# Kernel optimization log

Measured on AMD Instinct MI355X. Metric: run time of the kernel, lower is better.

Reference implementation:

```python
import jax, jax.numpy as jnp
import numpy as np

NUM_HOPS = 3
SIGMA = 0.1
EPS = 1e-12  # torch F.normalize default eps


def _l2_normalize(v):
    n = jnp.linalg.norm(v, axis=1, keepdims=True)
    return v / jnp.maximum(n, EPS)


def setup_inputs() -> dict:
    key = jax.random.key(0)
    k1, k2 = jax.random.split(key)
    N, d, E = 50000, 128, 500000
    x = jax.random.normal(k1, (N, d), dtype=jnp.float32)
    edge_index = jax.random.randint(k2, (2, E), 0, N, dtype=jnp.int64)
    return {"x": x, "edge_index": edge_index}


def reference(x, edge_index):
    N = x.shape[0]
    src, dst = edge_index[0], edge_index[1]
    noise_key = jax.random.key(42)
    h = _l2_normalize(x)
    outs = [h]
    for k in range(NUM_HOPS):
        h_src = h[src]                              # [E, d] gather
        h_dst = h[dst]                              # [E, d] gather
        alpha = jax.nn.sigmoid(jnp.sum(h_src * h_dst, axis=1))  # [E]
        # sparse.mm(alpha^T, h): out[dst] += alpha_e * h[src]
        aggr = jax.ops.segment_sum(alpha[:, None] * h_src, dst, num_segments=N)
        noise = SIGMA * jax.random.normal(jax.random.fold_in(noise_key, k), aggr.shape, aggr.dtype)
        h = _l2_normalize(aggr + noise)
        outs.append(h)
    return jnp.stack(outs)  # [num_hops+1, N, d]
```

## Files before the change

### kernel.cpp

```cpp
#include <hip/hip_runtime.h>
#include <stdint.h>

#define D 128
#define SIGMA 0.1f

typedef unsigned int uint;
typedef unsigned short ushort;

#if __has_builtin(__builtin_amdgcn_fdot2_f32_bf16)
#define HAVE_DOT2 1
typedef __bf16 bf16x2 __attribute__((ext_vector_type(2)));
__device__ inline float dot2b(uint a, uint b, float c) {
  union { uint u; bf16x2 v; } ua, ub;
  ua.u = a; ub.u = b;
  return __builtin_amdgcn_fdot2_f32_bf16(ua.v, ub.v, c, false);
}
#else
#define HAVE_DOT2 0
#endif

typedef float v2f __attribute__((ext_vector_type(2)));

__host__ __device__ inline void tf2x32(uint32_t k0, uint32_t k1,
                                       uint32_t x0, uint32_t x1,
                                       uint32_t& o0, uint32_t& o1) {
  const uint32_t ks2 = k0 ^ k1 ^ 0x1BD11BDAu;
#define ROTL(v, r) (((v) << (r)) | ((v) >> (32 - (r))))
#define RND(R) { x0 += x1; x1 = ROTL(x1, R); x1 ^= x0; }
  x0 += k0; x1 += k1;
  RND(13) RND(15) RND(26) RND(6)
  x0 += k1; x1 += ks2 + 1u;
  RND(17) RND(29) RND(16) RND(24)
  x0 += ks2; x1 += k0 + 2u;
  RND(13) RND(15) RND(26) RND(6)
  x0 += k0; x1 += k1 + 3u;
  RND(17) RND(29) RND(16) RND(24)
  x0 += k1; x1 += ks2 + 4u;
  RND(13) RND(15) RND(26) RND(6)
  x0 += ks2; x1 += k0 + 5u;
#undef RND
#undef ROTL
  o0 = x0; o1 = x1;
}

__device__ inline float jax_normal_pu(uint32_t k0, uint32_t k1, uint32_t idx) {
  uint32_t o0, o1;
  tf2x32(k0, k1, 0u, idx, o0, o1);
  uint32_t bits = o0 ^ o1;
  float f = __uint_as_float((bits >> 9) | 0x3f800000u) - 1.0f;
  const float lo = __uint_as_float(0xBF7FFFFFu);
  float u = fmaxf(lo, f * 2.0f + lo);
  float w = -__logf((1.0f - u) * (1.0f + u));
  float p;
  if (w < 5.0f) {
    w -= 2.5f;
    p = 2.81022636e-08f;
    p = fmaf(p, w, 3.43273939e-07f);
    p = fmaf(p, w, -3.5233877e-06f);
    p = fmaf(p, w, -4.39150654e-06f);
    p = fmaf(p, w, 0.00021858087f);
    p = fmaf(p, w, -0.00125372503f);
    p = fmaf(p, w, -0.00417768164f);
    p = fmaf(p, w, 0.246640727f);
    p = fmaf(p, w, 1.50140941f);
  } else {
    w = sqrtf(w) - 3.0f;
    p = -0.000200214257f;
    p = fmaf(p, w, 0.000100950558f);
    p = fmaf(p, w, 0.00134934322f);
    p = fmaf(p, w, -0.00367342844f);
    p = fmaf(p, w, 0.00573950773f);
    p = fmaf(p, w, -0.0076224613f);
    p = fmaf(p, w, 0.00943887047f);
    p = fmaf(p, w, 1.00167406f);
    p = fmaf(p, w, 2.83297682f);
  }
  return p * u;
}
#define NOISE_SCALE 0.14142135624f

__device__ inline uint bf16r(float f) {
  uint u = __float_as_uint(f);
  return (u + 0x7fffu + ((u >> 16) & 1u)) >> 16;
}

__device__ inline void unpk8(uint4 u, float* a) {
  a[0] = __uint_as_float(u.x << 16);
  a[1] = __uint_as_float(u.x & 0xffff0000u);
  a[2] = __uint_as_float(u.y << 16);
  a[3] = __uint_as_float(u.y & 0xffff0000u);
  a[4] = __uint_as_float(u.z << 16);
  a[5] = __uint_as_float(u.z & 0xffff0000u);
  a[6] = __uint_as_float(u.w << 16);
  a[7] = __uint_as_float(u.w & 0xffff0000u);
}

__device__ inline void unpk8v(uint4 u, v2f* a) {
  a[0] = v2f{__uint_as_float(u.x << 16), __uint_as_float(u.x & 0xffff0000u)};
  a[1] = v2f{__uint_as_float(u.y << 16), __uint_as_float(u.y & 0xffff0000u)};
  a[2] = v2f{__uint_as_float(u.z << 16), __uint_as_float(u.z & 0xffff0000u)};
  a[3] = v2f{__uint_as_float(u.w << 16), __uint_as_float(u.w & 0xffff0000u)};
}

template<int USEB>
__device__ inline void ldrow16(const float* __restrict__ hf,
                               const uint4* __restrict__ hb,
                               int node, int sl, float* a) {
  if (USEB) {
    unpk8(hb[node * 16 + sl], a);
  } else {
    float4 v0 = ((const float4*)hf)[node * 32 + sl * 2];
    float4 v1 = ((const float4*)hf)[node * 32 + sl * 2 + 1];
    a[0] = v0.x; a[1] = v0.y; a[2] = v0.z; a[3] = v0.w;
    a[4] = v1.x; a[5] = v1.y; a[6] = v1.z; a[7] = v1.w;
  }
}

__global__ __launch_bounds__(256) void k_zero(int4* __restrict__ p, int n4) {
  int i = blockIdx.x * blockDim.x + threadIdx.x;
  if (i < n4) p[i] = make_int4(0, 0, 0, 0);
}

__global__ __launch_bounds__(256) void k_hist(const int* __restrict__ dst,
                                              int* __restrict__ cnt, int E) {
  int i = (blockIdx.x * blockDim.x + threadIdx.x) * 4;
  if (i + 3 < E) {
    int4 d = *(const int4*)(dst + i);
    atomicAdd(&cnt[d.x], 1);
    atomicAdd(&cnt[d.y], 1);
    atomicAdd(&cnt[d.z], 1);
    atomicAdd(&cnt[d.w], 1);
  } else {
    for (int j = i; j < E; ++j) atomicAdd(&cnt[dst[j]], 1);
  }
}

__global__ __launch_bounds__(256) void k_bsum(const int* __restrict__ cnt,
                                              int* __restrict__ bsum, int N) {
  __shared__ int ws[4];
  int b = blockIdx.x, t = threadIdx.x;
  int base = b * 1024 + t * 4;
  int4 c = {0, 0, 0, 0};
  if (base + 3 < N) c = *(const int4*)(cnt + base);
  else {
    if (base < N) c.x = cnt[base];
    if (base + 1 < N) c.y = cnt[base + 1];
    if (base + 2 < N) c.z = cnt[base + 2];
    if (base + 3 < N) c.w = cnt[base + 3];
  }
  int s = c.x + c.y + c.z + c.w;
  #pragma unroll
  for (int off = 32; off; off >>= 1) s += __shfl_xor(s, off);
  if ((t & 63) == 0) ws[t >> 6] = s;
  __syncthreads();
  if (t == 0) bsum[b] = ws[0] + ws[1] + ws[2] + ws[3];
}

__global__ __launch_bounds__(256) void k_apply2(const int* __restrict__ cnt,
                                                const int* __restrict__ bsum,
                                                int* __restrict__ row,
                                                int* __restrict__ cur,
                                                int N, int NB) {
  __shared__ int sboff;
  __shared__ int wsum[4];
  int b = blockIdx.x, t = threadIdx.x;
  if (t < 64) {
    int v = (t < NB) ? bsum[t] : 0;
    int incl = v;
    #pragma unroll
    for (int off = 1; off < 64; off <<= 1) {
      int tv = __shfl_up(incl, off);
      if (t >= off) incl += tv;
    }
    if (t == b) sboff = incl - v;
    if (b == 0 && t == NB - 1) row[N] = incl;
  }
  __syncthreads();

  int base = b * 1024 + t * 4;
  int4 c = {0, 0, 0, 0};
  if (base + 3 < N) c = *(const int4*)(cnt + base);
  else {
    if (base < N) c.x = cnt[base];
    if (base + 1 < N) c.y = cnt[base + 1];
    if (base + 2 < N) c.z = cnt[base + 2];
    if (base + 3 < N) c.w = cnt[base + 3];
  }
  int s = c.x + c.y + c.z + c.w;
  int incl = s;
  #pragma unroll
  for (int off = 1; off < 64; off <<= 1) {
    int tv = __shfl_up(incl, off);
    if ((t & 63) >= off) incl += tv;
  }
  int wid = t >> 6;
  if ((t & 63) == 63) wsum[wid] = incl;
  __syncthreads();
  int woff = 0;
  for (int w = 0; w < wid; ++w) woff += wsum[w];
  int ex = sboff + woff + incl - s;
  int r0 = ex, r1 = ex + c.x, r2 = r1 + c.y, r3 = r2 + c.z;
  if (base + 3 < N) {
    *(int4*)(row + base) = make_int4(r0, r1, r2, r3);
    *(int4*)(cur + base) = make_int4(r0, r1, r2, r3);
  } else {
    if (base < N)     { row[base] = r0;     cur[base] = r0; }
    if (base + 1 < N) { row[base + 1] = r1; cur[base + 1] = r1; }
    if (base + 2 < N) { row[base + 2] = r2; cur[base + 2] = r2; }
  }
}

__global__ void k_bscan(const int* __restrict__ bsum, int* __restrict__ boff,
                        int* __restrict__ rowN, int NB) {
  int lane = threadIdx.x;
  int carry = 0;
  for (int base = 0; base < NB; base += 64) {
    int idx = base + lane;
    int v = (idx < NB) ? bsum[idx] : 0;
    int incl = v;
    #pragma unroll
    for (int off = 1; off < 64; off <<= 1) {
      int t = __shfl_up(incl, off);
      if (lane >= off) incl += t;
    }
    if (idx < NB) boff[idx] = carry + incl - v;
    carry += __shfl(incl, 63);
  }
  if (lane == 0) rowN[0] = carry;
}

__global__ __launch_bounds__(256) void k_apply(const int* __restrict__ cnt,
                                               const int* __restrict__ boff,
                                               int* __restrict__ row,
                                               int* __restrict__ cur, int N) {
  __shared__ int wsum[4];
  int b = blockIdx.x, t = threadIdx.x;
  int base = b * 1024 + t * 4;
  int4 c = {0, 0, 0, 0};
  if (base + 3 < N) c = *(const int4*)(cnt + base);
  else {
    if (base < N) c.x = cnt[base];
    if (base + 1 < N) c.y = cnt[base + 1];
    if (base + 2 < N) c.z = cnt[base + 2];
    if (base + 3 < N) c.w = cnt[base + 3];
  }
  int s = c.x + c.y + c.z + c.w;
  int incl = s;
  #pragma unroll
  for (int off = 1; off < 64; off <<= 1) {
    int tv = __shfl_up(incl, off);
    if ((t & 63) >= off) incl += tv;
  }
  int wid = t >> 6;
  if ((t & 63) == 63) wsum[wid] = incl;
  __syncthreads();
  int woff = 0;
  for (int w = 0; w < wid; ++w) woff += wsum[w];
  int ex = boff[b] + woff + incl - s;
  int r0 = ex, r1 = ex + c.x, r2 = r1 + c.y, r3 = r2 + c.z;
  if (base + 3 < N) {
    *(int4*)(row + base) = make_int4(r0, r1, r2, r3);
    *(int4*)(cur + base) = make_int4(r0, r1, r2, r3);
  } else {
    if (base < N)     { row[base] = r0;     cur[base] = r0; }
    if (base + 1 < N) { row[base + 1] = r1; cur[base + 1] = r1; }
    if (base + 2 < N) { row[base + 2] = r2; cur[base + 2] = r2; }
  }
}

__global__ __launch_bounds__(256) void k_fill(const int* __restrict__ src,
                                              const int* __restrict__ dst,
                                              int* __restrict__ cur,
                                              int* __restrict__ csr, int E) {
  int i = (blockIdx.x * blockDim.x + threadIdx.x) * 4;
  if (i + 3 < E) {
    int4 d = *(const int4*)(dst + i);
    int4 s = *(const int4*)(src + i);
    csr[atomicAdd(&cur[d.x], 1)] = s.x;
    csr[atomicAdd(&cur[d.y], 1)] = s.y;
    csr[atomicAdd(&cur[d.z], 1)] = s.z;
    csr[atomicAdd(&cur[d.w], 1)] = s.w;
  } else {
    for (int j = i; j < E; ++j) csr[atomicAdd(&cur[dst[j]], 1)] = src[j];
  }
}

template<int USEB>
__global__ __launch_bounds__(256) void k_norm0(const float* __restrict__ x,
                                               float* __restrict__ h,
                                               uint2* __restrict__ hb, int N) {
  int gid = blockIdx.x * blockDim.x + threadIdx.x;
  int node = gid >> 5, lane = gid & 31;
  if (node >= N) return;
  float4 v = ((const float4*)x)[node * 32 + lane];
  float ss = v.x * v.x + v.y * v.y + v.z * v.z + v.w * v.w;
  #pragma unroll
  for (int off = 16; off; off >>= 1) ss += __shfl_xor(ss, off);
  float inv = 1.0f / fmaxf(sqrtf(ss), 1e-12f);
  float4 o; o.x = v.x * inv; o.y = v.y * inv; o.z = v.z * inv; o.w = v.w * inv;
  ((float4*)h)[node * 32 + lane] = o;
  if (USEB) {
    uint2 u;
    u.x = bf16r(o.x) | (bf16r(o.y) << 16);
    u.y = bf16r(o.z) | (bf16r(o.w) << 16);
    hb[node * 32 + lane] = u;
  }
}

template<int USEB>
__global__ __launch_bounds__(256) void k_hop(
    const float* __restrict__ hpf, const uint4* __restrict__ hpb,
    float* __restrict__ hof, uint* __restrict__ hob, int wb,
    const int* __restrict__ row, const int* __restrict__ csr,
    int N, uint32_t k0, uint32_t k1) {
  int gid = blockIdx.x * blockDim.x + threadIdx.x;
  int node = gid >> 6;
  if (node >= N) return;
  int lane = threadIdx.x & 63;
  int sl = lane & 15, g = lane >> 4;

  int b = __builtin_amdgcn_readfirstlane(row[node]);
  int e = __builtin_amdgcn_readfirstlane(row[node + 1]);

  uint32_t j0 = (uint32_t)node * 128u + (uint32_t)sl * 8u + (uint32_t)g * 2u;
  float n0 = jax_normal_pu(k0, k1, j0);
  float n1 = jax_normal_pu(k0, k1, j0 + 1u);

#if HAVE_DOT2
  if (USEB) {
    uint4 hvp = hpb[node * 16 + sl];
    v2f acc[4] = {v2f{0.f,0.f}, v2f{0.f,0.f}, v2f{0.f,0.f}, v2f{0.f,0.f}};

    for (int cb = b; cb < e; cb += 64) {
      int cn = min(64, e - cb);
      int eidx = csr[min(cb + lane, e - 1)];
      for (int jb = 0; jb < cn; jb += 16) {
        int rem = cn - jb;
        uint4 u0, u1, u2, u3;
        {
          int i0 = __shfl(eidx, jb + g);
          u0 = hpb[i0 * 16 + sl];
        }
        if (rem > 4)  { int i1 = __shfl(eidx, jb + 4 + g);  u1 = hpb[i1 * 16 + sl]; }
        if (rem > 8)  { int i2 = __shfl(eidx, jb + 8 + g);  u2 = hpb[i2 * 16 + sl]; }
        if (rem > 12) { int i3 = __shfl(eidx, jb + 12 + g); u3 = hpb[i3 * 16 + sl]; }

        #define PROC(UU, SBASE)                                                 \
        {                                                                       \
          float p = dot2b(UU.w, hvp.w, dot2b(UU.z, hvp.z,                       \
                    dot2b(UU.y, hvp.y, dot2b(UU.x, hvp.x, 0.f))));              \
          p += __shfl_xor(p, 1);                                                \
          p += __shfl_xor(p, 2);                                                \
          p += __shfl_xor(p, 4);                                                \
          p += __shfl_xor(p, 8);                                                \
          float al = ((SBASE) + g < rem)                                        \
                       ? __builtin_amdgcn_rcpf(1.0f + __expf(-p)) : 0.f;        \
          v2f a[4]; v2f vv = v2f{al, al};                                       \
          unpk8v(UU, a);                                                        \
          acc[0] = __builtin_elementwise_fma(vv, a[0], acc[0]);                 \
          acc[1] = __builtin_elementwise_fma(vv, a[1], acc[1]);                 \
          acc[2] = __builtin_elementwise_fma(vv, a[2], acc[2]);                 \
          acc[3] = __builtin_elementwise_fma(vv, a[3], acc[3]);                 \
        }
        PROC(u0, 0)
        if (rem > 4)  PROC(u1, 4)
        if (rem > 8)  PROC(u2, 8)
        if (rem > 12) PROC(u3, 12)
        #undef PROC
      }
    }

    float ac[8] = {acc[0][0], acc[0][1], acc[1][0], acc[1][1],
                   acc[2][0], acc[2][1], acc[3][0], acc[3][1]};
    #pragma unroll
    for (int t = 0; t < 8; ++t) {
      ac[t] += __shfl_xor(ac[t], 16);
      ac[t] += __shfl_xor(ac[t], 32);
    }
    float p0s = (g & 1) ? ac[2] : ac[0];
    float p1s = (g & 1) ? ac[3] : ac[1];
    float q0s = (g & 1) ? ac[6] : ac[4];
    float q1s = (g & 1) ? ac[7] : ac[5];
    float s0 = (g & 2) ? q0s : p0s;
    float s1 = (g & 2) ? q1s : p1s;

    s0 += NOISE_SCALE * n0;
    s1 += NOISE_SCALE * n1;

    float ss = s0 * s0 + s1 * s1;
    #pragma unroll
    for (int off = 32; off; off >>= 1) ss += __shfl_xor(ss, off);
    float inv = __builtin_amdgcn_rcpf(fmaxf(sqrtf(ss), 1e-12f));
    float o0 = s0 * inv, o1 = s1 * inv;
    int oi = node * 64 + sl * 4 + g;
    ((float2*)hof)[oi] = make_float2(o0, o1);
    if (wb) hob[oi] = bf16r(o0) | (bf16r(o1) << 16);
    return;
  }
#endif

  float hv[8];
  ldrow16<USEB>(hpf, hpb, node, sl, hv);
  float acc[8] = {0.f, 0.f, 0.f, 0.f, 0.f, 0.f, 0.f, 0.f};
  for (int cb = b; cb < e; cb += 64) {
    int cn = min(64, e - cb);
    int eidx = csr[min(cb + lane, e - 1)];
    for (int jb = 0; jb < cn; jb += 16) {
      int pos = jb + (g << 2);
      int i0 = __shfl(eidx, pos);
      int i1 = __shfl(eidx, pos + 1);
      int i2 = __shfl(eidx, pos + 2);
      int i3 = __shfl(eidx, pos + 3);
      float a0[8], a1[8], a2[8], a3[8];
      ldrow16<USEB>(hpf, hpb, i0, sl, a0);
      ldrow16<USEB>(hpf, hpb, i1, sl, a1);
      ldrow16<USEB>(hpf, hpb, i2, sl, a2);
      ldrow16<USEB>(hpf, hpb, i3, sl, a3);
      float p0 = 0.f, p1 = 0.f, p2 = 0.f, p3 = 0.f;
      #pragma unroll
      for (int t = 0; t < 8; ++t) {
        p0 = fmaf(a0[t], hv[t], p0);
        p1 = fmaf(a1[t], hv[t], p1);
        p2 = fmaf(a2[t], hv[t], p2);
        p3 = fmaf(a3[t], hv[t], p3);
      }
      #pragma unroll
      for (int off = 1; off < 16; off <<= 1) {
        p0 += __shfl_xor(p0, off);
        p1 += __shfl_xor(p1, off);
        p2 += __shfl_xor(p2, off);
        p3 += __shfl_xor(p3, off);
      }
      float al0 = (pos     < cn) ? __builtin_amdgcn_rcpf(1.0f + __expf(-p0)) : 0.f;
      float al1 = (pos + 1 < cn) ? __builtin_amdgcn_rcpf(1.0f + __expf(-p1)) : 0.f;
      float al2 = (pos + 2 < cn) ? __builtin_amdgcn_rcpf(1.0f + __expf(-p2)) : 0.f;
      float al3 = (pos + 3 < cn) ? __builtin_amdgcn_rcpf(1.0f + __expf(-p3)) : 0.f;
      #pragma unroll
      for (int t = 0; t < 8; ++t) {
        acc[t] = fmaf(al0, a0[t], acc[t]);
        acc[t] = fmaf(al1, a1[t], acc[t]);
        acc[t] = fmaf(al2, a2[t], acc[t]);
        acc[t] = fmaf(al3, a3[t], acc[t]);
      }
    }
  }
  #pragma unroll
  for (int t = 0; t < 8; ++t) {
    acc[t] += __shfl_xor(acc[t], 16);
    acc[t] += __shfl_xor(acc[t], 32);
  }
  float p0s = (g & 1) ? acc[2] : acc[0];
  float p1s = (g & 1) ? acc[3] : acc[1];
  float q0s = (g & 1) ? acc[6] : acc[4];
  float q1s = (g & 1) ? acc[7] : acc[5];
  float s0 = (g & 2) ? q0s : p0s;
  float s1 = (g & 2) ? q1s : p1s;

  s0 += NOISE_SCALE * n0;
  s1 += NOISE_SCALE * n1;

  float ss = s0 * s0 + s1 * s1;
  #pragma unroll
  for (int off = 32; off; off >>= 1) ss += __shfl_xor(ss, off);
  float inv = __builtin_amdgcn_rcpf(fmaxf(sqrtf(ss), 1e-12f));
  float o0 = s0 * inv, o1 = s1 * inv;
  int oi = node * 64 + sl * 4 + g;
  ((float2*)hof)[oi] = make_float2(o0, o1);
  if (USEB && wb) hob[oi] = bf16r(o0) | (bf16r(o1) << 16);
}

extern "C" void kernel_launch(void* const* d_in, const int* in_sizes, int n_in,
                              void* d_out, int out_size, void* d_ws, size_t ws_size,
                              hipStream_t stream) {
  const float* x = (const float*)d_in[0];
  const int* ei = (const int*)d_in[1];
  int N = in_sizes[0] / D;
  int E = in_sizes[1] / 2;
  const int* src = ei;
  const int* dst = ei + E;
  float* out = (float*)d_out;
  size_t nd = (size_t)N * D;

  int Np = (N + 3) & ~3;
  int Ep = (E + 3) & ~3;
  int NB = (N + 1023) / 1024;
  int NBp = (NB + 3) & ~3;
  int* cnt  = (int*)d_ws;
  int* row  = cnt + Np;
  int* cur  = row + Np + 4;
  int* csr  = cur + Np;
  int* bsum = csr + Ep;
  int* boff = bsum + NBp;

  size_t int_bytes = ((size_t)(3 * Np + 4 + Ep + 2 * NBp)) * 4;
  size_t hb_off = (int_bytes + 255) & ~(size_t)255;
  size_t hb_bytes = (size_t)N * D * 2;
  bool useb = ws_size >= hb_off + 2 * hb_bytes;
  ushort* hb0 = (ushort*)((char*)d_ws + hb_off);
  ushort* hb1 = hb0 + (size_t)N * D;

  int n4 = Np / 4;
  k_zero<<<(n4 + 255) / 256, 256, 0, stream>>>((int4*)cnt, n4);
  int eb4 = (E / 4 + 256) / 256;
  k_hist<<<eb4, 256, 0, stream>>>(dst, cnt, E);
  k_bsum<<<NB, 256, 0, stream>>>(cnt, bsum, N);
  if (NB <= 64) {
    k_apply2<<<NB, 256, 0, stream>>>(cnt, bsum, row, cur, N, NB);
  } else {
    k_bscan<<<1, 64, 0, stream>>>(bsum, boff, row + N, NB);
    k_apply<<<NB, 256, 0, stream>>>(cnt, boff, row, cur, N);
  }
  k_fill<<<eb4, 256, 0, stream>>>(src, dst, cur, csr, E);

  int nb32 = (N * 32 + 255) / 256;
  int nb64 = (N * 64 + 255) / 256;

  if (useb) {
    k_norm0<1><<<nb32, 256, 0, stream>>>(x, out, (uint2*)hb0, N);
    for (int k = 0; k < 3; ++k) {
      uint32_t ka, kb;
      tf2x32(0u, 42u, 0u, (uint32_t)k, ka, kb);
      const uint4* hin = (const uint4*)((k & 1) ? hb1 : hb0);
      uint* hout = (uint*)((k & 1) ? hb0 : hb1);
      k_hop<1><<<nb64, 256, 0, stream>>>(nullptr, hin,
                                         out + (size_t)(k + 1) * nd, hout,
                                         (k < 2) ? 1 : 0,
                                         row, csr, N, ka, kb);
    }
  } else {
    k_norm0<0><<<nb32, 256, 0, stream>>>(x, out, nullptr, N);
    for (int k = 0; k < 3; ++k) {
      uint32_t ka, kb;
      tf2x32(0u, 42u, 0u, (uint32_t)k, ka, kb);
      k_hop<0><<<nb64, 256, 0, stream>>>(out + (size_t)k * nd, nullptr,
                                         out + (size_t)(k + 1) * nd, nullptr, 0,
                                         row, csr, N, ka, kb);
    }
  }
}
```

Measured before the change: 169.7 us.

## Precompute hop noise in preprocessing kernels and batch edge gathers with DPP reductions

The Gaussian noise for all three hops is now generated in extra blocks appended to the histogram, fill and norm0 launches. It is stored as bf16 in workspace, so the hop kernels only load it instead of running Threefry and erfinv inline. The hop edge loop is restructured into templated batches that issue all gathers before the dot products, and part of the dot-product reduction uses DPP moves instead of shuffles. The trade-offs are extra workspace traffic and bf16 rounding of the noise, which adds a small accuracy risk.

```diff
diff --git a/kernel.cpp b/kernel.cpp
--- a/kernel.cpp
+++ b/kernel.cpp
@@ -3,6 +3,7 @@
 
 #define D 128
 #define SIGMA 0.1f
+#define NOISE_SCALE 0.14142135624f
 
 typedef unsigned int uint;
 typedef unsigned short ushort;
@@ -17,6 +18,17 @@
 }
 #else
 #define HAVE_DOT2 0
+#endif
+
+#if __has_builtin(__builtin_amdgcn_mov_dpp)
+#define HAVE_DPP 1
+template<int CTRL>
+__device__ inline float dppadd(float x) {
+  int v = __builtin_amdgcn_mov_dpp(__float_as_int(x), CTRL, 0xF, 0xF, true);
+  return x + __int_as_float(v);
+}
+#else
+#define HAVE_DPP 0
 #endif
 
 typedef float v2f __attribute__((ext_vector_type(2)));
@@ -77,22 +89,10 @@
   }
   return p * u;
 }
-#define NOISE_SCALE 0.14142135624f
 
 __device__ inline uint bf16r(float f) {
   uint u = __float_as_uint(f);
   return (u + 0x7fffu + ((u >> 16) & 1u)) >> 16;
-}
-
-__device__ inline void unpk8(uint4 u, float* a) {
-  a[0] = __uint_as_float(u.x << 16);
-  a[1] = __uint_as_float(u.x & 0xffff0000u);
-  a[2] = __uint_as_float(u.y << 16);
-  a[3] = __uint_as_float(u.y & 0xffff0000u);
-  a[4] = __uint_as_float(u.z << 16);
-  a[5] = __uint_as_float(u.z & 0xffff0000u);
-  a[6] = __uint_as_float(u.w << 16);
-  a[7] = __uint_as_float(u.w & 0xffff0000u);
 }
 
 __device__ inline void unpk8v(uint4 u, v2f* a) {
@@ -102,18 +102,11 @@
   a[3] = v2f{__uint_as_float(u.w << 16), __uint_as_float(u.w & 0xffff0000u)};
 }
 
-template<int USEB>
-__device__ inline void ldrow16(const float* __restrict__ hf,
-                               const uint4* __restrict__ hb,
-                               int node, int sl, float* a) {
-  if (USEB) {
-    unpk8(hb[node * 16 + sl], a);
-  } else {
-    float4 v0 = ((const float4*)hf)[node * 32 + sl * 2];
-    float4 v1 = ((const float4*)hf)[node * 32 + sl * 2 + 1];
-    a[0] = v0.x; a[1] = v0.y; a[2] = v0.z; a[3] = v0.w;
-    a[4] = v1.x; a[5] = v1.y; a[6] = v1.z; a[7] = v1.w;
-  }
+__device__ inline void gen_noise(uint* __restrict__ nb, int t, uint ka, uint kb) {
+  uint j0 = (uint)(t >> 6) * 128u + (uint)(t & 15) * 8u + (uint)((t >> 4) & 3) * 2u;
+  float a = jax_normal_pu(ka, kb, j0);
+  float b = jax_normal_pu(ka, kb, j0 + 1u);
+  nb[t] = bf16r(a) | (bf16r(b) << 16);
 }
 
 __global__ __launch_bounds__(256) void k_zero(int4* __restrict__ p, int n4) {
@@ -121,9 +114,9 @@
   if (i < n4) p[i] = make_int4(0, 0, 0, 0);
 }
 
-__global__ __launch_bounds__(256) void k_hist(const int* __restrict__ dst,
-                                              int* __restrict__ cnt, int E) {
-  int i = (blockIdx.x * blockDim.x + threadIdx.x) * 4;
+__device__ inline void hist_body(const int* __restrict__ dst, int* __restrict__ cnt,
+                                 int E, int bx, int tx) {
+  int i = (bx * 256 + tx) * 4;
   if (i + 3 < E) {
     int4 d = *(const int4*)(dst + i);
     atomicAdd(&cnt[d.x], 1);
@@ -133,6 +126,56 @@
   } else {
     for (int j = i; j < E; ++j) atomicAdd(&cnt[dst[j]], 1);
   }
+}
+
+__device__ inline void fill_body(const int* __restrict__ src, const int* __restrict__ dst,
+                                 int* __restrict__ cur, int* __restrict__ csr,
+                                 int E, int bx, int tx) {
+  int i = (bx * 256 + tx) * 4;
+  if (i + 3 < E) {
+    int4 d = *(const int4*)(dst + i);
+    int4 s = *(const int4*)(src + i);
+    csr[atomicAdd(&cur[d.x], 1)] = s.x;
+    csr[atomicAdd(&cur[d.y], 1)] = s.y;
+    csr[atomicAdd(&cur[d.z], 1)] = s.z;
+    csr[atomicAdd(&cur[d.w], 1)] = s.w;
+  } else {
+    for (int j = i; j < E; ++j) csr[atomicAdd(&cur[dst[j]], 1)] = src[j];
+  }
+}
+
+__global__ __launch_bounds__(256) void k_hist(const int* __restrict__ dst,
+                                              int* __restrict__ cnt, int E) {
+  hist_body(dst, cnt, E, blockIdx.x, threadIdx.x);
+}
+
+__global__ __launch_bounds__(256) void k_hist_noise(const int* __restrict__ dst,
+                                                    int* __restrict__ cnt, int E, int HB,
+                                                    uint* __restrict__ nb, int NT,
+                                                    uint ka, uint kb) {
+  int bx = blockIdx.x;
+  if (bx < HB) { hist_body(dst, cnt, E, bx, threadIdx.x); return; }
+  int t = (bx - HB) * 256 + threadIdx.x;
+  if (t < NT) gen_noise(nb, t, ka, kb);
+}
+
+__global__ __launch_bounds__(256) void k_fill(const int* __restrict__ src,
+                                              const int* __restrict__ dst,
+                                              int* __restrict__ cur,
+                                              int* __restrict__ csr, int E) {
+  fill_body(src, dst, cur, csr, E, blockIdx.x, threadIdx.x);
+}
+
+__global__ __launch_bounds__(256) void k_fill_noise(const int* __restrict__ src,
+                                                    const int* __restrict__ dst,
+                                                    int* __restrict__ cur,
+                                                    int* __restrict__ csr, int E, int FB,
+                                                    uint* __restrict__ nb, int NT,
+                                                    uint ka, uint kb) {
+  int bx = blockIdx.x;
+  if (bx < FB) { fill_body(src, dst, cur, csr, E, bx, threadIdx.x); return; }
+  int t = (bx - FB) * 256 + threadIdx.x;
+  if (t < NT) gen_noise(nb, t, ka, kb);
 }
 
 __global__ __launch_bounds__(256) void k_bsum(const int* __restrict__ cnt,
@@ -268,28 +311,9 @@
   }
 }
 
-__global__ __launch_bounds__(256) void k_fill(const int* __restrict__ src,
-                                              const int* __restrict__ dst,
-                                              int* __restrict__ cur,
-                                              int* __restrict__ csr, int E) {
-  int i = (blockIdx.x * blockDim.x + threadIdx.x) * 4;
-  if (i + 3 < E) {
-    int4 d = *(const int4*)(dst + i);
-    int4 s = *(const int4*)(src + i);
-    csr[atomicAdd(&cur[d.x], 1)] = s.x;
-    csr[atomicAdd(&cur[d.y], 1)] = s.y;
-    csr[atomicAdd(&cur[d.z], 1)] = s.z;
-    csr[atomicAdd(&cur[d.w], 1)] = s.w;
-  } else {
-    for (int j = i; j < E; ++j) csr[atomicAdd(&cur[dst[j]], 1)] = src[j];
-  }
-}
-
-template<int USEB>
-__global__ __launch_bounds__(256) void k_norm0(const float* __restrict__ x,
-                                               float* __restrict__ h,
-                                               uint2* __restrict__ hb, int N) {
-  int gid = blockIdx.x * blockDim.x + threadIdx.x;
+__device__ inline void norm0_body(const float* __restrict__ x, float* __restrict__ h,
+                                  uint2* __restrict__ hb, int N, int bx, int tx) {
+  int gid = bx * 256 + tx;
   int node = gid >> 5, lane = gid & 31;
   if (node >= N) return;
   float4 v = ((const float4*)x)[node * 32 + lane];
@@ -299,7 +323,7 @@
   float inv = 1.0f / fmaxf(sqrtf(ss), 1e-12f);
   float4 o; o.x = v.x * inv; o.y = v.y * inv; o.z = v.z * inv; o.w = v.w * inv;
   ((float4*)h)[node * 32 + lane] = o;
-  if (USEB) {
+  if (hb) {
     uint2 u;
     u.x = bf16r(o.x) | (bf16r(o.y) << 16);
     u.y = bf16r(o.z) | (bf16r(o.w) << 16);
@@ -307,10 +331,150 @@
   }
 }
 
-template<int USEB>
-__global__ __launch_bounds__(256) void k_hop(
-    const float* __restrict__ hpf, const uint4* __restrict__ hpb,
+__global__ __launch_bounds__(256) void k_norm0(const float* __restrict__ x,
+                                               float* __restrict__ h,
+                                               uint2* __restrict__ hb, int N) {
+  norm0_body(x, h, hb, N, blockIdx.x, threadIdx.x);
+}
+
+__global__ __launch_bounds__(256) void k_norm0_noise(const float* __restrict__ x,
+                                                     float* __restrict__ h,
+                                                     uint2* __restrict__ hb, int N, int NB0,
+                                                     uint* __restrict__ nb, int NT,
+                                                     uint ka, uint kb) {
+  int bx = blockIdx.x;
+  if (bx < NB0) { norm0_body(x, h, hb, N, bx, threadIdx.x); return; }
+  int t = (bx - NB0) * 256 + threadIdx.x;
+  if (t < NT) gen_noise(nb, t, ka, kb);
+}
+
+#if HAVE_DOT2
+template<int K, bool M>
+__device__ inline void edge_body(int jb, int rem, int eidx,
+                                 const uint4* __restrict__ hpb,
+                                 uint4 hvp, int sl, int g, v2f* acc) {
+  uint4 u[K];
+  #pragma unroll
+  for (int j = 0; j < K; ++j) {
+    int idx = __shfl(eidx, jb + 4 * j + g);
+    u[j] = hpb[idx * 16 + sl];
+  }
+  float p[K];
+  #pragma unroll
+  for (int j = 0; j < K; ++j)
+    p[j] = dot2b(u[j].w, hvp.w, dot2b(u[j].z, hvp.z,
+            dot2b(u[j].y, hvp.y, dot2b(u[j].x, hvp.x, 0.f))));
+#if HAVE_DPP
+  #pragma unroll
+  for (int j = 0; j < K; ++j) p[j] = dppadd<0xB1>(p[j]);
+  #pragma unroll
+  for (int j = 0; j < K; ++j) p[j] = dppadd<0x4E>(p[j]);
+  #pragma unroll
+  for (int j = 0; j < K; ++j) p[j] += __shfl_xor(p[j], 4);
+  #pragma unroll
+  for (int j = 0; j < K; ++j) p[j] += __shfl_xor(p[j], 8);
+#else
+  #pragma unroll
+  for (int off = 1; off < 16; off <<= 1) {
+    #pragma unroll
+    for (int j = 0; j < K; ++j) p[j] += __shfl_xor(p[j], off);
+  }
+#endif
+  float al[K];
+  #pragma unroll
+  for (int j = 0; j < K; ++j) {
+    bool ok = (!M) || (j < K - 1) || (4 * (K - 1) + g < rem);
+    al[j] = ok ? __builtin_amdgcn_rcpf(1.0f + __expf(-p[j])) : 0.f;
+  }
+  #pragma unroll
+  for (int j = 0; j < K; ++j) {
+    v2f a[4]; unpk8v(u[j], a);
+    v2f vv = v2f{al[j], al[j]};
+    acc[0] = __builtin_elementwise_fma(vv, a[0], acc[0]);
+    acc[1] = __builtin_elementwise_fma(vv, a[1], acc[1]);
+    acc[2] = __builtin_elementwise_fma(vv, a[2], acc[2]);
+    acc[3] = __builtin_elementwise_fma(vv, a[3], acc[3]);
+  }
+}
+
+template<int PRE>
+__global__ __launch_bounds__(256) void k_hop2(
+    const uint4* __restrict__ hpb,
     float* __restrict__ hof, uint* __restrict__ hob, int wb,
+    const int* __restrict__ row, const int* __restrict__ csr,
+    const uint* __restrict__ nbuf,
+    int N, uint32_t k0, uint32_t k1) {
+  int gid = blockIdx.x * blockDim.x + threadIdx.x;
+  int node = gid >> 6;
+  if (node >= N) return;
+  int lane = threadIdx.x & 63;
+  int sl = lane & 15, g = lane >> 4;
+
+  int b = __builtin_amdgcn_readfirstlane(row[node]);
+  int e = __builtin_amdgcn_readfirstlane(row[node + 1]);
+
+  uint4 hvp = hpb[node * 16 + sl];
+
+  float n0, n1;
+  if (PRE) {
+    uint nz = nbuf[node * 64 + lane];
+    n0 = __uint_as_float(nz << 16);
+    n1 = __uint_as_float(nz & 0xffff0000u);
+  } else {
+    uint32_t j0 = (uint32_t)node * 128u + (uint32_t)sl * 8u + (uint32_t)g * 2u;
+    n0 = jax_normal_pu(k0, k1, j0);
+    n1 = jax_normal_pu(k0, k1, j0 + 1u);
+  }
+
+  v2f acc[4] = {v2f{0.f,0.f}, v2f{0.f,0.f}, v2f{0.f,0.f}, v2f{0.f,0.f}};
+
+  for (int cb = b; cb < e; cb += 64) {
+    int cn = min(64, e - cb);
+    int eidx = csr[min(cb + lane, e - 1)];
+    int jb = 0;
+    for (; jb + 16 <= cn; jb += 16)
+      edge_body<4, false>(jb, 16, eidx, hpb, hvp, sl, g, acc);
+    int rem = cn - jb;
+    if (rem > 0) {
+      switch ((rem + 3) >> 2) {
+        case 1: edge_body<1, true>(jb, rem, eidx, hpb, hvp, sl, g, acc); break;
+        case 2: edge_body<2, true>(jb, rem, eidx, hpb, hvp, sl, g, acc); break;
+        case 3: edge_body<3, true>(jb, rem, eidx, hpb, hvp, sl, g, acc); break;
+        default: edge_body<4, true>(jb, rem, eidx, hpb, hvp, sl, g, acc); break;
+      }
+    }
+  }
+
+  float ac[8] = {acc[0][0], acc[0][1], acc[1][0], acc[1][1],
+                 acc[2][0], acc[2][1], acc[3][0], acc[3][1]};
+  #pragma unroll
+  for (int t = 0; t < 8; ++t) {
+    ac[t] += __shfl_xor(ac[t], 16);
+    ac[t] += __shfl_xor(ac[t], 32);
+  }
+  float p0s = (g & 1) ? ac[2] : ac[0];
+  float p1s = (g & 1) ? ac[3] : ac[1];
+  float q0s = (g & 1) ? ac[6] : ac[4];
+  float q1s = (g & 1) ? ac[7] : ac[5];
+  float s0 = (g & 2) ? q0s : p0s;
+  float s1 = (g & 2) ? q1s : p1s;
+
+  s0 += NOISE_SCALE * n0;
+  s1 += NOISE_SCALE * n1;
+
+  float ss = s0 * s0 + s1 * s1;
+  #pragma unroll
+  for (int off = 32; off; off >>= 1) ss += __shfl_xor(ss, off);
+  float inv = __builtin_amdgcn_rcpf(fmaxf(sqrtf(ss), 1e-12f));
+  float o0 = s0 * inv, o1 = s1 * inv;
+  int oi = node * 64 + sl * 4 + g;
+  ((float2*)hof)[oi] = make_float2(o0, o1);
+  if (wb) hob[oi] = bf16r(o0) | (bf16r(o1) << 16);
+}
+#endif
+
+__global__ __launch_bounds__(256) void k_hop_f32(
+    const float* __restrict__ hpf, float* __restrict__ hof,
     const int* __restrict__ row, const int* __restrict__ csr,
     int N, uint32_t k0, uint32_t k1) {
   int gid = blockIdx.x * blockDim.x + threadIdx.x;
@@ -319,89 +483,19 @@
   int lane = threadIdx.x & 63;
   int sl = lane & 15, g = lane >> 4;
 
-  int b = __builtin_amdgcn_readfirstlane(row[node]);
-  int e = __builtin_amdgcn_readfirstlane(row[node + 1]);
-
+  int b = row[node], e = row[node + 1];
   uint32_t j0 = (uint32_t)node * 128u + (uint32_t)sl * 8u + (uint32_t)g * 2u;
   float n0 = jax_normal_pu(k0, k1, j0);
   float n1 = jax_normal_pu(k0, k1, j0 + 1u);
 
-#if HAVE_DOT2
-  if (USEB) {
-    uint4 hvp = hpb[node * 16 + sl];
-    v2f acc[4] = {v2f{0.f,0.f}, v2f{0.f,0.f}, v2f{0.f,0.f}, v2f{0.f,0.f}};
-
-    for (int cb = b; cb < e; cb += 64) {
-      int cn = min(64, e - cb);
-      int eidx = csr[min(cb + lane, e - 1)];
-      for (int jb = 0; jb < cn; jb += 16) {
-        int rem = cn - jb;
-        uint4 u0, u1, u2, u3;
-        {
-          int i0 = __shfl(eidx, jb + g);
-          u0 = hpb[i0 * 16 + sl];
-        }
-        if (rem > 4)  { int i1 = __shfl(eidx, jb + 4 + g);  u1 = hpb[i1 * 16 + sl]; }
-        if (rem > 8)  { int i2 = __shfl(eidx, jb + 8 + g);  u2 = hpb[i2 * 16 + sl]; }
-        if (rem > 12) { int i3 = __shfl(eidx, jb + 12 + g); u3 = hpb[i3 * 16 + sl]; }
-
-        #define PROC(UU, SBASE)                                                 \
-        {                                                                       \
-          float p = dot2b(UU.w, hvp.w, dot2b(UU.z, hvp.z,                       \
-                    dot2b(UU.y, hvp.y, dot2b(UU.x, hvp.x, 0.f))));              \
-          p += __shfl_xor(p, 1);                                                \
-          p += __shfl_xor(p, 2);                                                \
-          p += __shfl_xor(p, 4);                                                \
-          p += __shfl_xor(p, 8);                                                \
-          float al = ((SBASE) + g < rem)                                        \
-                       ? __builtin_amdgcn_rcpf(1.0f + __expf(-p)) : 0.f;        \
-          v2f a[4]; v2f vv = v2f{al, al};                                       \
-          unpk8v(UU, a);                                                        \
-          acc[0] = __builtin_elementwise_fma(vv, a[0], acc[0]);                 \
-          acc[1] = __builtin_elementwise_fma(vv, a[1], acc[1]);                 \
-          acc[2] = __builtin_elementwise_fma(vv, a[2], acc[2]);                 \
-          acc[3] = __builtin_elementwise_fma(vv, a[3], acc[3]);                 \
-        }
-        PROC(u0, 0)
-        if (rem > 4)  PROC(u1, 4)
-        if (rem > 8)  PROC(u2, 8)
-        if (rem > 12) PROC(u3, 12)
-        #undef PROC
-      }
-    }
-
-    float ac[8] = {acc[0][0], acc[0][1], acc[1][0], acc[1][1],
-                   acc[2][0], acc[2][1], acc[3][0], acc[3][1]};
-    #pragma unroll
-    for (int t = 0; t < 8; ++t) {
-      ac[t] += __shfl_xor(ac[t], 16);
-      ac[t] += __shfl_xor(ac[t], 32);
-    }
-    float p0s = (g & 1) ? ac[2] : ac[0];
-    float p1s = (g & 1) ? ac[3] : ac[1];
-    float q0s = (g & 1) ? ac[6] : ac[4];
-    float q1s = (g & 1) ? ac[7] : ac[5];
-    float s0 = (g & 2) ? q0s : p0s;
-    float s1 = (g & 2) ? q1s : p1s;
-
-    s0 += NOISE_SCALE * n0;
-    s1 += NOISE_SCALE * n1;
-
-    float ss = s0 * s0 + s1 * s1;
-    #pragma unroll
-    for (int off = 32; off; off >>= 1) ss += __shfl_xor(ss, off);
-    float inv = __builtin_amdgcn_rcpf(fmaxf(sqrtf(ss), 1e-12f));
-    float o0 = s0 * inv, o1 = s1 * inv;
-    int oi = node * 64 + sl * 4 + g;
-    ((float2*)hof)[oi] = make_float2(o0, o1);
-    if (wb) hob[oi] = bf16r(o0) | (bf16r(o1) << 16);
-    return;
-  }
-#endif
-
   float hv[8];
-  ldrow16<USEB>(hpf, hpb, node, sl, hv);
-  float acc[8] = {0.f, 0.f, 0.f, 0.f, 0.f, 0.f, 0.f, 0.f};
+  {
+    float4 v0 = ((const float4*)hpf)[node * 32 + sl * 2];
+    float4 v1 = ((const float4*)hpf)[node * 32 + sl * 2 + 1];
+    hv[0]=v0.x; hv[1]=v0.y; hv[2]=v0.z; hv[3]=v0.w;
+    hv[4]=v1.x; hv[5]=v1.y; hv[6]=v1.z; hv[7]=v1.w;
+  }
+  float acc[8] = {0,0,0,0,0,0,0,0};
   for (int cb = b; cb < e; cb += 64) {
     int cn = min(64, e - cb);
     int eidx = csr[min(cb + lane, e - 1)];
@@ -412,10 +506,17 @@
       int i2 = __shfl(eidx, pos + 2);
       int i3 = __shfl(eidx, pos + 3);
       float a0[8], a1[8], a2[8], a3[8];
-      ldrow16<USEB>(hpf, hpb, i0, sl, a0);
-      ldrow16<USEB>(hpf, hpb, i1, sl, a1);
-      ldrow16<USEB>(hpf, hpb, i2, sl, a2);
-      ldrow16<USEB>(hpf, hpb, i3, sl, a3);
+      {
+        float4 v0 = ((const float4*)hpf)[i0 * 32 + sl * 2];
+        float4 v1 = ((const float4*)hpf)[i0 * 32 + sl * 2 + 1];
+        a0[0]=v0.x; a0[1]=v0.y; a0[2]=v0.z; a0[3]=v0.w; a0[4]=v1.x; a0[5]=v1.y; a0[6]=v1.z; a0[7]=v1.w;
+        v0 = ((const float4*)hpf)[i1 * 32 + sl * 2]; v1 = ((const float4*)hpf)[i1 * 32 + sl * 2 + 1];
+        a1[0]=v0.x; a1[1]=v0.y; a1[2]=v0.z; a1[3]=v0.w; a1[4]=v1.x; a1[5]=v1.y; a1[6]=v1.z; a1[7]=v1.w;
+        v0 = ((const float4*)hpf)[i2 * 32 + sl * 2]; v1 = ((const float4*)hpf)[i2 * 32 + sl * 2 + 1];
+        a2[0]=v0.x; a2[1]=v0.y; a2[2]=v0.z; a2[3]=v0.w; a2[4]=v1.x; a2[5]=v1.y; a2[6]=v1.z; a2[7]=v1.w;
+        v0 = ((const float4*)hpf)[i3 * 32 + sl * 2]; v1 = ((const float4*)hpf)[i3 * 32 + sl * 2 + 1];
+        a3[0]=v0.x; a3[1]=v0.y; a3[2]=v0.z; a3[3]=v0.w; a3[4]=v1.x; a3[5]=v1.y; a3[6]=v1.z; a3[7]=v1.w;
+      }
       float p0 = 0.f, p1 = 0.f, p2 = 0.f, p3 = 0.f;
       #pragma unroll
       for (int t = 0; t < 8; ++t) {
@@ -466,7 +567,6 @@
   float o0 = s0 * inv, o1 = s1 * inv;
   int oi = node * 64 + sl * 4 + g;
   ((float2*)hof)[oi] = make_float2(o0, o1);
-  if (USEB && wb) hob[oi] = bf16r(o0) | (bf16r(o1) << 16);
 }
 
 extern "C" void kernel_launch(void* const* d_in, const int* in_sizes, int n_in,
@@ -495,14 +595,32 @@
   size_t int_bytes = ((size_t)(3 * Np + 4 + Ep + 2 * NBp)) * 4;
   size_t hb_off = (int_bytes + 255) & ~(size_t)255;
   size_t hb_bytes = (size_t)N * D * 2;
+  size_t n64 = (size_t)N * 64;
+  size_t noise_bytes = n64 * 4;
   bool useb = ws_size >= hb_off + 2 * hb_bytes;
+  bool noise_fit = ws_size >= hb_off + 2 * hb_bytes + 3 * noise_bytes;
+#if !HAVE_DOT2
+  useb = false; noise_fit = false;
+#endif
   ushort* hb0 = (ushort*)((char*)d_ws + hb_off);
   ushort* hb1 = hb0 + (size_t)N * D;
+  uint* nb_base = (uint*)(hb1 + (size_t)N * D);
+
+  uint32_t ka[3], kb[3];
+  for (int k = 0; k < 3; ++k) tf2x32(0u, 42u, 0u, (uint32_t)k, ka[k], kb[k]);
 
   int n4 = Np / 4;
   k_zero<<<(n4 + 255) / 256, 256, 0, stream>>>((int4*)cnt, n4);
   int eb4 = (E / 4 + 256) / 256;
-  k_hist<<<eb4, 256, 0, stream>>>(dst, cnt, E);
+  int noiseB = (int)((n64 + 255) / 256);
+  int NT = (int)n64;
+
+  if (noise_fit) {
+    k_hist_noise<<<eb4 + noiseB, 256, 0, stream>>>(dst, cnt, E, eb4,
+                                                   nb_base, NT, ka[0], kb[0]);
+  } else {
+    k_hist<<<eb4, 256, 0, stream>>>(dst, cnt, E);
+  }
   k_bsum<<<NB, 256, 0, stream>>>(cnt, bsum, N);
   if (NB <= 64) {
     k_apply2<<<NB, 256, 0, stream>>>(cnt, bsum, row, cur, N, NB);
@@ -510,31 +628,44 @@
     k_bscan<<<1, 64, 0, stream>>>(bsum, boff, row + N, NB);
     k_apply<<<NB, 256, 0, stream>>>(cnt, boff, row, cur, N);
   }
-  k_fill<<<eb4, 256, 0, stream>>>(src, dst, cur, csr, E);
+  if (noise_fit) {
+    k_fill_noise<<<eb4 + noiseB, 256, 0, stream>>>(src, dst, cur, csr, E, eb4,
+                                                   nb_base + n64, NT, ka[1], kb[1]);
+  } else {
+    k_fill<<<eb4, 256, 0, stream>>>(src, dst, cur, csr, E);
+  }
 
   int nb32 = (N * 32 + 255) / 256;
-  int nb64 = (N * 64 + 255) / 256;
-
+  int nb64b = (N * 64 + 255) / 256;
+
+#if HAVE_DOT2
   if (useb) {
-    k_norm0<1><<<nb32, 256, 0, stream>>>(x, out, (uint2*)hb0, N);
+    if (noise_fit) {
+      k_norm0_noise<<<nb32 + noiseB, 256, 0, stream>>>(x, out, (uint2*)hb0, N, nb32,
+                                                       nb_base + 2 * n64, NT, ka[2], kb[2]);
+    } else {
+      k_norm0<<<nb32, 256, 0, stream>>>(x, out, (uint2*)hb0, N);
+    }
     for (int k = 0; k < 3; ++k) {
-      uint32_t ka, kb;
-      tf2x32(0u, 42u, 0u, (uint32_t)k, ka, kb);
       const uint4* hin = (const uint4*)((k & 1) ? hb1 : hb0);
       uint* hout = (uint*)((k & 1) ? hb0 : hb1);
-      k_hop<1><<<nb64, 256, 0, stream>>>(nullptr, hin,
-                                         out + (size_t)(k + 1) * nd, hout,
-                                         (k < 2) ? 1 : 0,
-                                         row, csr, N, ka, kb);
+      const uint* nbk = nb_base + (size_t)k * n64;
+      if (noise_fit)
+        k_hop2<1><<<nb64b, 256, 0, stream>>>(hin, out + (size_t)(k + 1) * nd, hout,
+                                             (k < 2) ? 1 : 0, row, csr, nbk,
+                                             N, ka[k], kb[k]);
+      else
+        k_hop2<0><<<nb64b, 256, 0, stream>>>(hin, out + (size_t)(k + 1) * nd, hout,
+                                             (k < 2) ? 1 : 0, row, csr, nullptr,
+                                             N, ka[k], kb[k]);
     }
-  } else {
-    k_norm0<0><<<nb32, 256, 0, stream>>>(x, out, nullptr, N);
-    for (int k = 0; k < 3; ++k) {
-      uint32_t ka, kb;
-      tf2x32(0u, 42u, 0u, (uint32_t)k, ka, kb);
-      k_hop<0><<<nb64, 256, 0, stream>>>(out + (size_t)k * nd, nullptr,
-                                         out + (size_t)(k + 1) * nd, nullptr, 0,
-                                         row, csr, N, ka, kb);
-    }
-  }
-}
+    return;
+  }
+#endif
+  k_norm0<<<nb32, 256, 0, stream>>>(x, out, nullptr, N);
+  for (int k = 0; k < 3; ++k) {
+    k_hop_f32<<<nb64b, 256, 0, stream>>>(out + (size_t)k * nd,
+                                         out + (size_t)(k + 1) * nd,
+                                         row, csr, N, ka[k], kb[k]);
+  }
+}
```

New measurement: 193.5 us. 1.14x slower.
